# Optimization experiments

Hardware: AMD Instinct MI355X
Metric: run time of the kernel (lower is better)

## Reference

```python
import jax, jax.numpy as jnp
import numpy as np

IN_FEATURES = 4096
OUT_FEATURES = 8192
LUT_SIZE = 65536  # 256 * 256 two-level codebook


def setup_inputs() -> dict:
    key = jax.random.key(0)
    k_x, k_b, k_f, k_s, k_l = jax.random.split(key, 5)
    x = jax.random.normal(k_x, (2, 256, IN_FEATURES), dtype=jnp.float32)
    base_idx = jax.random.randint(k_b, (OUT_FEATURES, IN_FEATURES), 0, 256, dtype=jnp.int32)
    fine_idx = jax.random.randint(k_f, (OUT_FEATURES, IN_FEATURES), 0, 256, dtype=jnp.int32)
    scale = jax.random.uniform(k_s, (OUT_FEATURES, 1), dtype=jnp.float32)
    lut = jax.random.normal(k_l, (LUT_SIZE,), dtype=jnp.float32)
    return {"x": x, "base_idx": base_idx, "fine_idx": fine_idx, "scale": scale, "lut": lut}


def reference(x, base_idx, fine_idx, scale, lut):
    # Two-level LUT dequant: combined 16-bit index = base*256 + fine
    combined_idx = base_idx * 256 + fine_idx              # [out, in] int32
    weights = lut[combined_idx] * scale                   # [out, in] fp32, per-row scale
    # F.linear(x, weights) == x @ weights.T
    return jnp.einsum('bsi,oi->bso', x, weights)
```

## Files before the change

kernel.cpp:

```cpp
#include <hip/hip_runtime.h>

typedef unsigned short ushort_t;
typedef unsigned int   uint32;
typedef __attribute__((ext_vector_type(8)))  short short8;
typedef __attribute__((ext_vector_type(4)))  float floatx4;
typedef __attribute__((ext_vector_type(16))) float floatx16;
typedef __attribute__((ext_vector_type(4)))  int   intx4;
typedef __attribute__((ext_vector_type(4)))  float fltx4;

#define IN_F   4096
#define OUT_F  8192
#define M_TOT  512

__device__ __forceinline__ ushort_t f2bf(float f) {
    uint32 u = __builtin_bit_cast(uint32, f);
    u += 0x7FFFu + ((u >> 16) & 1u);
    return (ushort_t)(u >> 16);
}
__device__ __forceinline__ uint32 pack2bf(float a, float b) {
    return (uint32)f2bf(a) | ((uint32)f2bf(b) << 16);
}

__global__ void cvt_x_kernel(const float* __restrict__ x, ushort_t* __restrict__ xb) {
    const int g  = blockIdx.x * 256 + threadIdx.x;
    const int r  = g >> 9;
    const int k0 = (g & 511) * 8;
    float4 v0 = *(const float4*)(x + (size_t)r * IN_F + k0);
    float4 v1 = *(const float4*)(x + (size_t)r * IN_F + k0 + 4);
    short8 s;
    s[0] = (short)f2bf(v0.x); s[1] = (short)f2bf(v0.y);
    s[2] = (short)f2bf(v0.z); s[3] = (short)f2bf(v0.w);
    s[4] = (short)f2bf(v1.x); s[5] = (short)f2bf(v1.y);
    s[6] = (short)f2bf(v1.z); s[7] = (short)f2bf(v1.w);
    const int mt = r >> 5;
    const int kt = k0 >> 4;
    ushort_t* dst = xb + ((size_t)(mt * 256 + kt) * 32 + (r & 31)) * 16 + (k0 & 15);
    *(short8*)dst = s;
}

__global__ __launch_bounds__(1024, 4)
void fused_kernel(const ushort_t* __restrict__ xb, const int* __restrict__ base_idx,
                  const int* __restrict__ fine_idx, const float* __restrict__ lut,
                  const float* __restrict__ scale, float* __restrict__ out)
{
    __shared__ ushort_t sh_lut[65536];
    __shared__ ushort_t sh_w[3][32 * 128];

    const int tid  = threadIdx.x;
    const int nblk = blockIdx.x;

    for (int i = tid * 4; i < 65536; i += 4096) {
        fltx4 v = __builtin_nontemporal_load((const fltx4*)(lut + i));
        *(uint32*)&sh_lut[i]     = pack2bf(v.x, v.y);
        *(uint32*)&sh_lut[i + 2] = pack2bf(v.z, v.w);
    }

    const int colr = tid >> 5;
    const int kq   = (tid & 31) * 4;
    const intx4* bp = (const intx4*)(base_idx + (size_t)(nblk * 32 + colr) * IN_F + kq);
    const intx4* fp = (const intx4*)(fine_idx + (size_t)(nblk * 32 + colr) * IN_F + kq);

    const int woff = colr * 128 + (((kq >> 3) ^ (colr & 7)) << 3) + (kq & 7);

    const int lane = tid & 63;
    const int wave = tid >> 6;
    const int l31  = lane & 31;
    const int lhi  = lane >> 5;
    const int rx8  = l31 & 7;

    const ushort_t* abase = xb + (size_t)wave * 256 * 512 + l31 * 16 + lhi * 8;

    intx4 i0b = __builtin_nontemporal_load(bp);
    intx4 i0f = __builtin_nontemporal_load(fp);
    intx4 i1b = __builtin_nontemporal_load(bp + 32);
    intx4 i1f = __builtin_nontemporal_load(fp + 32);
    intx4 Ib  = __builtin_nontemporal_load(bp + 64);
    intx4 If  = __builtin_nontemporal_load(fp + 64);
    intx4 Nb  = __builtin_nontemporal_load(bp + 96);
    intx4 Nf  = __builtin_nontemporal_load(fp + 96);
    intx4 Pb = {0, 0, 0, 0}, Pf = {0, 0, 0, 0};

    short8 aA[8], aB[8];
#pragma unroll
    for (int i = 0; i < 8; ++i)
        aA[i] = *(const short8*)(abase + (size_t)i * 512);

    asm volatile("s_waitcnt lgkmcnt(0)" ::: "memory");
    __builtin_amdgcn_sched_barrier(0);
    __builtin_amdgcn_s_barrier();

    {
        uint32 w0 = (uint32)sh_lut[(i0b.x << 8) + i0f.x]
                  | ((uint32)sh_lut[(i0b.y << 8) + i0f.y] << 16);
        uint32 w1 = (uint32)sh_lut[(i0b.z << 8) + i0f.z]
                  | ((uint32)sh_lut[(i0b.w << 8) + i0f.w] << 16);
        uint2 wv; wv.x = w0; wv.y = w1;
        *(uint2*)&sh_w[0][woff] = wv;
        w0 = (uint32)sh_lut[(i1b.x << 8) + i1f.x]
           | ((uint32)sh_lut[(i1b.y << 8) + i1f.y] << 16);
        w1 = (uint32)sh_lut[(i1b.z << 8) + i1f.z]
           | ((uint32)sh_lut[(i1b.w << 8) + i1f.w] << 16);
        wv.x = w0; wv.y = w1;
        *(uint2*)&sh_w[1][woff] = wv;
    }

    asm volatile("s_waitcnt lgkmcnt(0)" ::: "memory");
    __builtin_amdgcn_sched_barrier(0);
    __builtin_amdgcn_s_barrier();

    floatx16 acc = {0.f,0.f,0.f,0.f,0.f,0.f,0.f,0.f,0.f,0.f,0.f,0.f,0.f,0.f,0.f,0.f};

#define GBODY(K, AX, AY, CUR, WD)                                              \
    {                                                                          \
        const int T = t + (K);                                                 \
        if (T + 4 < 32) {                                                      \
            Pb = __builtin_nontemporal_load(bp + (T + 4) * 32);                \
            Pf = __builtin_nontemporal_load(fp + (T + 4) * 32);                \
        }                                                                      \
        if (T + 1 < 32) {                                                      \
            _Pragma("unroll")                                                  \
            for (int i = 0; i < 8; ++i)                                        \
                AY[i] = *(const short8*)(abase + (size_t)((T + 1) * 8 + i) * 512); \
        }                                                                      \
        const ushort_t* wb = sh_w[CUR];                                        \
        __builtin_amdgcn_s_setprio(1);                                         \
        _Pragma("unroll")                                                      \
        for (int i = 0; i < 8; ++i) {                                          \
            short8 bfr = *(const short8*)&wb[l31 * 128 + (((2 * i + lhi) ^ rx8) << 3)]; \
            acc = __builtin_amdgcn_mfma_f32_32x32x16_bf16(AX[i], bfr, acc, 0, 0, 0);    \
        }                                                                      \
        __builtin_amdgcn_s_setprio(0);                                         \
        if (T + 2 < 32) {                                                      \
            uint32 w0 = (uint32)sh_lut[(Ib.x << 8) + If.x]                     \
                      | ((uint32)sh_lut[(Ib.y << 8) + If.y] << 16);            \
            uint32 w1 = (uint32)sh_lut[(Ib.z << 8) + If.z]                     \
                      | ((uint32)sh_lut[(Ib.w << 8) + If.w] << 16);            \
            uint2 wv; wv.x = w0; wv.y = w1;                                    \
            *(uint2*)&sh_w[WD][woff] = wv;                                     \
            Ib = Nb; If = Nf; Nb = Pb; Nf = Pf;                                \
        }                                                                      \
        __builtin_amdgcn_sched_barrier(0);                                     \
        __builtin_amdgcn_s_barrier();                                          \
    }

    int t = 0;
    for (; t < 30; t += 6) {
        GBODY(0, aA, aB, 0, 2)
        GBODY(1, aB, aA, 1, 0)
        GBODY(2, aA, aB, 2, 1)
        GBODY(3, aB, aA, 0, 2)
        GBODY(4, aA, aB, 1, 0)
        GBODY(5, aB, aA, 2, 1)
    }
    GBODY(0, aA, aB, 0, 2)
    GBODY(1, aB, aA, 1, 0)
#undef GBODY

    const float sc = scale[nblk * 32 + l31];
    float* op = out + (size_t)(nblk * 32 + l31);
    const int rbase = wave * 32 + 4 * lhi;
#pragma unroll
    for (int reg = 0; reg < 16; ++reg) {
        const int row = rbase + (reg & 3) + 8 * (reg >> 2);
        op[(size_t)row * OUT_F] = acc[reg] * sc;
    }
}

#define NB  32
#define FBK 128
#define WS  136
#define NITER (IN_F / FBK)
__global__ __launch_bounds__(1024, 4)
void ghost_kernel(const float* __restrict__ xf,
                  const int* __restrict__ base_idx, const int* __restrict__ fine_idx,
                  const float* __restrict__ scale, const float* __restrict__ lut,
                  float* __restrict__ out)
{
    __shared__ ushort_t sh_lut[65536];
    __shared__ ushort_t sh_w[2][NB * WS];
    const int tid = threadIdx.x;
    const int n0  = blockIdx.x * NB;
    for (int i = tid * 4; i < 65536; i += 1024 * 4) {
        float4 v = *(const float4*)(lut + i);
        sh_lut[i + 0] = f2bf(v.x); sh_lut[i + 1] = f2bf(v.y);
        sh_lut[i + 2] = f2bf(v.z); sh_lut[i + 3] = f2bf(v.w);
    }
    const int sn  = tid >> 5;
    const int skq = (tid & 31) * 4;
    const int* bp = base_idx + (size_t)(n0 + sn) * IN_F + skq;
    const int* fp = fine_idx + (size_t)(n0 + sn) * IN_F + skq;
    __syncthreads();
    int4 pb = *(const int4*)(bp);
    int4 pf = *(const int4*)(fp);
    {
        uint32 w0 = (uint32)sh_lut[(pb.x << 8) + pf.x] | ((uint32)sh_lut[(pb.y << 8) + pf.y] << 16);
        uint32 w1 = (uint32)sh_lut[(pb.z << 8) + pf.z] | ((uint32)sh_lut[(pb.w << 8) + pf.w] << 16);
        uint2 wv; wv.x = w0; wv.y = w1;
        *(uint2*)&sh_w[0][sn * WS + skq] = wv;
    }
    pb = *(const int4*)(bp + FBK);
    pf = *(const int4*)(fp + FBK);
    __syncthreads();
    const int lane = tid & 63;
    const int wave = tid >> 6;
    const int l16  = lane & 15;
    const int quad = lane >> 4;
    floatx4 acc[2][2];
    const floatx4 zero = {0.f, 0.f, 0.f, 0.f};
    acc[0][0] = zero; acc[0][1] = zero; acc[1][0] = zero; acc[1][1] = zero;
    const int mrow = wave * 32 + l16;
    const float* xrowf = xf + (size_t)mrow * IN_F + quad * 8;
    for (int t = 0; t < NITER; ++t) {
        const int k0 = t * FBK;
        {
            uint32 w0 = (uint32)sh_lut[(pb.x << 8) + pf.x] | ((uint32)sh_lut[(pb.y << 8) + pf.y] << 16);
            uint32 w1 = (uint32)sh_lut[(pb.z << 8) + pf.z] | ((uint32)sh_lut[(pb.w << 8) + pf.w] << 16);
            uint2 wv; wv.x = w0; wv.y = w1;
            *(uint2*)&sh_w[(t + 1) & 1][sn * WS + skq] = wv;
        }
        {
            const int kk = (t + 2 < NITER ? t + 2 : NITER - 1) * FBK;
            pb = *(const int4*)(bp + kk);
            pf = *(const int4*)(fp + kk);
        }
        const ushort_t* wb = sh_w[t & 1];
#pragma unroll
        for (int ks = 0; ks < 4; ++ks) {
            const int kk = k0 + ks * 32;
            short8 b0 = *(const short8*)&wb[l16        * WS + ks * 32 + quad * 8];
            short8 b1 = *(const short8*)&wb[(16 + l16) * WS + ks * 32 + quad * 8];
            short8 a0, a1;
            const float* p0 = xrowf + kk;
            const float* p1 = xrowf + (size_t)16 * IN_F + kk;
            float4 u0 = *(const float4*)p0, u1 = *(const float4*)(p0 + 4);
            float4 v0 = *(const float4*)p1, v1 = *(const float4*)(p1 + 4);
            a0[0] = (short)f2bf(u0.x); a0[1] = (short)f2bf(u0.y);
            a0[2] = (short)f2bf(u0.z); a0[3] = (short)f2bf(u0.w);
            a0[4] = (short)f2bf(u1.x); a0[5] = (short)f2bf(u1.y);
            a0[6] = (short)f2bf(u1.z); a0[7] = (short)f2bf(u1.w);
            a1[0] = (short)f2bf(v0.x); a1[1] = (short)f2bf(v0.y);
            a1[2] = (short)f2bf(v0.z); a1[3] = (short)f2bf(v0.w);
            a1[4] = (short)f2bf(v1.x); a1[5] = (short)f2bf(v1.y);
            a1[6] = (short)f2bf(v1.z); a1[7] = (short)f2bf(v1.w);
            acc[0][0] = __builtin_amdgcn_mfma_f32_16x16x32_bf16(a0, b0, acc[0][0], 0, 0, 0);
            acc[0][1] = __builtin_amdgcn_mfma_f32_16x16x32_bf16(a0, b1, acc[0][1], 0, 0, 0);
            acc[1][0] = __builtin_amdgcn_mfma_f32_16x16x32_bf16(a1, b0, acc[1][0], 0, 0, 0);
            acc[1][1] = __builtin_amdgcn_mfma_f32_16x16x32_bf16(a1, b1, acc[1][1], 0, 0, 0);
        }
        __syncthreads();
    }
#pragma unroll
    for (int nf = 0; nf < 2; ++nf) {
        const int col = n0 + nf * 16 + l16;
        const float sc = scale[col];
#pragma unroll
        for (int f = 0; f < 2; ++f) {
            const int r0 = wave * 32 + f * 16 + quad * 4;
#pragma unroll
            for (int r = 0; r < 4; ++r) {
                out[(size_t)(r0 + r) * OUT_F + col] = acc[f][nf][r] * sc;
            }
        }
    }
}

extern "C" void kernel_launch(void* const* d_in, const int* in_sizes, int n_in,
                              void* d_out, int out_size, void* d_ws, size_t ws_size,
                              hipStream_t stream) {
    const float* x      = (const float*)d_in[0];
    const int*   bidx   = (const int*)d_in[1];
    const int*   fidx   = (const int*)d_in[2];
    const float* scale  = (const float*)d_in[3];
    const float* lut    = (const float*)d_in[4];
    float*       out    = (float*)d_out;

    const size_t xb_bytes = (size_t)M_TOT * IN_F * sizeof(ushort_t);

    if (ws_size >= xb_bytes) {
        ushort_t* xbuf = (ushort_t*)d_ws;
        cvt_x_kernel<<<1024, 256, 0, stream>>>(x, xbuf);
        fused_kernel<<<256, 1024, 0, stream>>>(xbuf, bidx, fidx, lut, scale, out);
    } else {
        ghost_kernel<<<OUT_F / NB, 1024, 0, stream>>>(x, bidx, fidx, scale, lut, out);
    }
}
```

Baseline: 327.3 us.

## Halve block to 512 threads with two M-tiles per wave

The fused kernel now runs 512 threads instead of 1024. Each wave computes two 32-row M tiles with two accumulators, so every B fragment read from LDS feeds two MFMAs. Each thread now dequantizes 8 weights per stage with 16-byte LDS stores instead of 4, which halves the number of barrier participants and the LDS B-read traffic per MFMA. In exchange, register pressure roughly doubles from the duplicated A fragments and accumulators, and fewer waves are left to hide LUT gather latency.

```diff
diff --git a/kernel.cpp b/kernel.cpp
--- a/kernel.cpp
+++ b/kernel.cpp
@@ -38,7 +38,7 @@
     *(short8*)dst = s;
 }
 
-__global__ __launch_bounds__(1024, 4)
+__global__ __launch_bounds__(512, 2)
 void fused_kernel(const ushort_t* __restrict__ xb, const int* __restrict__ base_idx,
                   const int* __restrict__ fine_idx, const float* __restrict__ lut,
                   const float* __restrict__ scale, float* __restrict__ out)
@@ -49,18 +49,18 @@
     const int tid  = threadIdx.x;
     const int nblk = blockIdx.x;
 
-    for (int i = tid * 4; i < 65536; i += 4096) {
+    for (int i = tid * 4; i < 65536; i += 2048) {
         fltx4 v = __builtin_nontemporal_load((const fltx4*)(lut + i));
         *(uint32*)&sh_lut[i]     = pack2bf(v.x, v.y);
         *(uint32*)&sh_lut[i + 2] = pack2bf(v.z, v.w);
     }
 
-    const int colr = tid >> 5;
-    const int kq   = (tid & 31) * 4;
-    const intx4* bp = (const intx4*)(base_idx + (size_t)(nblk * 32 + colr) * IN_F + kq);
-    const intx4* fp = (const intx4*)(fine_idx + (size_t)(nblk * 32 + colr) * IN_F + kq);
-
-    const int woff = colr * 128 + (((kq >> 3) ^ (colr & 7)) << 3) + (kq & 7);
+    const int colr = tid >> 4;
+    const int koct = (tid & 15) * 8;
+    const intx4* bp = (const intx4*)(base_idx + (size_t)(nblk * 32 + colr) * IN_F + koct);
+    const intx4* fp = (const intx4*)(fine_idx + (size_t)(nblk * 32 + colr) * IN_F + koct);
+
+    const int woff = colr * 128 + (((tid & 15) ^ (colr & 7)) << 3);
 
     const int lane = tid & 63;
     const int wave = tid >> 6;
@@ -68,76 +68,90 @@
     const int lhi  = lane >> 5;
     const int rx8  = l31 & 7;
 
-    const ushort_t* abase = xb + (size_t)wave * 256 * 512 + l31 * 16 + lhi * 8;
-
-    intx4 i0b = __builtin_nontemporal_load(bp);
-    intx4 i0f = __builtin_nontemporal_load(fp);
-    intx4 i1b = __builtin_nontemporal_load(bp + 32);
-    intx4 i1f = __builtin_nontemporal_load(fp + 32);
-    intx4 Ib  = __builtin_nontemporal_load(bp + 64);
-    intx4 If  = __builtin_nontemporal_load(fp + 64);
-    intx4 Nb  = __builtin_nontemporal_load(bp + 96);
-    intx4 Nf  = __builtin_nontemporal_load(fp + 96);
-    intx4 Pb = {0, 0, 0, 0}, Pf = {0, 0, 0, 0};
-
-    short8 aA[8], aB[8];
-#pragma unroll
-    for (int i = 0; i < 8; ++i)
-        aA[i] = *(const short8*)(abase + (size_t)i * 512);
+    const ushort_t* abase = xb + (size_t)(wave * 2) * 256 * 512 + l31 * 16 + lhi * 8;
+
+    intx4 i0bA = __builtin_nontemporal_load(bp);
+    intx4 i0bB = __builtin_nontemporal_load(bp + 1);
+    intx4 i0fA = __builtin_nontemporal_load(fp);
+    intx4 i0fB = __builtin_nontemporal_load(fp + 1);
+    intx4 i1bA = __builtin_nontemporal_load(bp + 32);
+    intx4 i1bB = __builtin_nontemporal_load(bp + 33);
+    intx4 i1fA = __builtin_nontemporal_load(fp + 32);
+    intx4 i1fB = __builtin_nontemporal_load(fp + 33);
+    intx4 IbA  = __builtin_nontemporal_load(bp + 64);
+    intx4 IbB  = __builtin_nontemporal_load(bp + 65);
+    intx4 IfA  = __builtin_nontemporal_load(fp + 64);
+    intx4 IfB  = __builtin_nontemporal_load(fp + 65);
+    intx4 NbA  = __builtin_nontemporal_load(bp + 96);
+    intx4 NbB  = __builtin_nontemporal_load(bp + 97);
+    intx4 NfA  = __builtin_nontemporal_load(fp + 96);
+    intx4 NfB  = __builtin_nontemporal_load(fp + 97);
+
+    short8 aA0[8], aA1[8], aB0[8], aB1[8];
+#pragma unroll
+    for (int i = 0; i < 8; ++i) {
+        aA0[i] = *(const short8*)(abase + (size_t)i * 512);
+        aA1[i] = *(const short8*)(abase + 131072 + (size_t)i * 512);
+    }
 
     asm volatile("s_waitcnt lgkmcnt(0)" ::: "memory");
     __builtin_amdgcn_sched_barrier(0);
     __builtin_amdgcn_s_barrier();
 
-    {
-        uint32 w0 = (uint32)sh_lut[(i0b.x << 8) + i0f.x]
-                  | ((uint32)sh_lut[(i0b.y << 8) + i0f.y] << 16);
-        uint32 w1 = (uint32)sh_lut[(i0b.z << 8) + i0f.z]
-                  | ((uint32)sh_lut[(i0b.w << 8) + i0f.w] << 16);
-        uint2 wv; wv.x = w0; wv.y = w1;
-        *(uint2*)&sh_w[0][woff] = wv;
-        w0 = (uint32)sh_lut[(i1b.x << 8) + i1f.x]
-           | ((uint32)sh_lut[(i1b.y << 8) + i1f.y] << 16);
-        w1 = (uint32)sh_lut[(i1b.z << 8) + i1f.z]
-           | ((uint32)sh_lut[(i1b.w << 8) + i1f.w] << 16);
-        wv.x = w0; wv.y = w1;
-        *(uint2*)&sh_w[1][woff] = wv;
-    }
+#define DEQ8(BA, BB, FA, FB, DST)                                              \
+    {                                                                          \
+        uint32 w0 = (uint32)sh_lut[((BA).x << 8) + (FA).x]                     \
+                  | ((uint32)sh_lut[((BA).y << 8) + (FA).y] << 16);            \
+        uint32 w1 = (uint32)sh_lut[((BA).z << 8) + (FA).z]                     \
+                  | ((uint32)sh_lut[((BA).w << 8) + (FA).w] << 16);            \
+        uint32 w2 = (uint32)sh_lut[((BB).x << 8) + (FB).x]                     \
+                  | ((uint32)sh_lut[((BB).y << 8) + (FB).y] << 16);            \
+        uint32 w3 = (uint32)sh_lut[((BB).z << 8) + (FB).z]                     \
+                  | ((uint32)sh_lut[((BB).w << 8) + (FB).w] << 16);            \
+        uint4 wv; wv.x = w0; wv.y = w1; wv.z = w2; wv.w = w3;                  \
+        *(uint4*)(DST) = wv;                                                   \
+    }
+
+    DEQ8(i0bA, i0bB, i0fA, i0fB, &sh_w[0][woff])
+    DEQ8(i1bA, i1bB, i1fA, i1fB, &sh_w[1][woff])
 
     asm volatile("s_waitcnt lgkmcnt(0)" ::: "memory");
     __builtin_amdgcn_sched_barrier(0);
     __builtin_amdgcn_s_barrier();
 
-    floatx16 acc = {0.f,0.f,0.f,0.f,0.f,0.f,0.f,0.f,0.f,0.f,0.f,0.f,0.f,0.f,0.f,0.f};
-
-#define GBODY(K, AX, AY, CUR, WD)                                              \
+    const floatx16 z16 = {0.f,0.f,0.f,0.f,0.f,0.f,0.f,0.f,0.f,0.f,0.f,0.f,0.f,0.f,0.f,0.f};
+    floatx16 acc0 = z16, acc1 = z16;
+
+#define GBODY(K, AX0, AX1, AY0, AY1, CUR, WD)                                  \
     {                                                                          \
         const int T = t + (K);                                                 \
+        intx4 PbA = {0,0,0,0}, PbB = {0,0,0,0}, PfA = {0,0,0,0}, PfB = {0,0,0,0}; \
         if (T + 4 < 32) {                                                      \
-            Pb = __builtin_nontemporal_load(bp + (T + 4) * 32);                \
-            Pf = __builtin_nontemporal_load(fp + (T + 4) * 32);                \
+            PbA = __builtin_nontemporal_load(bp + (T + 4) * 32);               \
+            PbB = __builtin_nontemporal_load(bp + (T + 4) * 32 + 1);           \
+            PfA = __builtin_nontemporal_load(fp + (T + 4) * 32);               \
+            PfB = __builtin_nontemporal_load(fp + (T + 4) * 32 + 1);           \
         }                                                                      \
         if (T + 1 < 32) {                                                      \
             _Pragma("unroll")                                                  \
-            for (int i = 0; i < 8; ++i)                                        \
-                AY[i] = *(const short8*)(abase + (size_t)((T + 1) * 8 + i) * 512); \
+            for (int i = 0; i < 8; ++i) {                                      \
+                AY0[i] = *(const short8*)(abase + (size_t)((T + 1) * 8 + i) * 512); \
+                AY1[i] = *(const short8*)(abase + 131072 + (size_t)((T + 1) * 8 + i) * 512); \
+            }                                                                  \
         }                                                                      \
         const ushort_t* wb = sh_w[CUR];                                        \
         __builtin_amdgcn_s_setprio(1);                                         \
         _Pragma("unroll")                                                      \
-        for (int i = 0; i < 8; ++i) {                                          \
-            short8 bfr = *(const short8*)&wb[l31 * 128 + (((2 * i + lhi) ^ rx8) << 3)]; \
-            acc = __builtin_amdgcn_mfma_f32_32x32x16_bf16(AX[i], bfr, acc, 0, 0, 0);    \
+        for (int ks = 0; ks < 8; ++ks) {                                       \
+            short8 bfr = *(const short8*)&wb[l31 * 128 + (((2 * ks + lhi) ^ rx8) << 3)]; \
+            acc0 = __builtin_amdgcn_mfma_f32_32x32x16_bf16(AX0[ks], bfr, acc0, 0, 0, 0); \
+            acc1 = __builtin_amdgcn_mfma_f32_32x32x16_bf16(AX1[ks], bfr, acc1, 0, 0, 0); \
         }                                                                      \
         __builtin_amdgcn_s_setprio(0);                                         \
         if (T + 2 < 32) {                                                      \
-            uint32 w0 = (uint32)sh_lut[(Ib.x << 8) + If.x]                     \
-                      | ((uint32)sh_lut[(Ib.y << 8) + If.y] << 16);            \
-            uint32 w1 = (uint32)sh_lut[(Ib.z << 8) + If.z]                     \
-                      | ((uint32)sh_lut[(Ib.w << 8) + If.w] << 16);            \
-            uint2 wv; wv.x = w0; wv.y = w1;                                    \
-            *(uint2*)&sh_w[WD][woff] = wv;                                     \
-            Ib = Nb; If = Nf; Nb = Pb; Nf = Pf;                                \
+            DEQ8(IbA, IbB, IfA, IfB, &sh_w[WD][woff])                          \
+            IbA = NbA; IbB = NbB; IfA = NfA; IfB = NfB;                        \
+            NbA = PbA; NbB = PbB; NfA = PfA; NfB = PfB;                        \
         }                                                                      \
         __builtin_amdgcn_sched_barrier(0);                                     \
         __builtin_amdgcn_s_barrier();                                          \
@@ -145,24 +159,29 @@
 
     int t = 0;
     for (; t < 30; t += 6) {
-        GBODY(0, aA, aB, 0, 2)
-        GBODY(1, aB, aA, 1, 0)
-        GBODY(2, aA, aB, 2, 1)
-        GBODY(3, aB, aA, 0, 2)
-        GBODY(4, aA, aB, 1, 0)
-        GBODY(5, aB, aA, 2, 1)
-    }
-    GBODY(0, aA, aB, 0, 2)
-    GBODY(1, aB, aA, 1, 0)
+        GBODY(0, aA0, aA1, aB0, aB1, 0, 2)
+        GBODY(1, aB0, aB1, aA0, aA1, 1, 0)
+        GBODY(2, aA0, aA1, aB0, aB1, 2, 1)
+        GBODY(3, aB0, aB1, aA0, aA1, 0, 2)
+        GBODY(4, aA0, aA1, aB0, aB1, 1, 0)
+        GBODY(5, aB0, aB1, aA0, aA1, 2, 1)
+    }
+    GBODY(0, aA0, aA1, aB0, aB1, 0, 2)
+    GBODY(1, aB0, aB1, aA0, aA1, 1, 0)
 #undef GBODY
+#undef DEQ8
 
     const float sc = scale[nblk * 32 + l31];
     float* op = out + (size_t)(nblk * 32 + l31);
-    const int rbase = wave * 32 + 4 * lhi;
-#pragma unroll
-    for (int reg = 0; reg < 16; ++reg) {
-        const int row = rbase + (reg & 3) + 8 * (reg >> 2);
-        op[(size_t)row * OUT_F] = acc[reg] * sc;
+#pragma unroll
+    for (int mt = 0; mt < 2; ++mt) {
+        const floatx16 a = mt ? acc1 : acc0;
+        const int rbase = (wave * 2 + mt) * 32 + 4 * lhi;
+#pragma unroll
+        for (int reg = 0; reg < 16; ++reg) {
+            const int row = rbase + (reg & 3) + 8 * (reg >> 2);
+            op[(size_t)row * OUT_F] = a[reg] * sc;
+        }
     }
 }
 
@@ -279,7 +298,7 @@
     if (ws_size >= xb_bytes) {
         ushort_t* xbuf = (ushort_t*)d_ws;
         cvt_x_kernel<<<1024, 256, 0, stream>>>(x, xbuf);
-        fused_kernel<<<256, 1024, 0, stream>>>(xbuf, bidx, fidx, lut, scale, out);
+        fused_kernel<<<256, 512, 0, stream>>>(xbuf, bidx, fidx, lut, scale, out);
     } else {
         ghost_kernel<<<OUT_F / NB, 1024, 0, stream>>>(x, bidx, fidx, scale, lut, out);
     }
```

After: 326.9 us. About the same (-0.1%).
